# Kernel tuning notes

Hardware: AMD Instinct MI355X
Metric: run time of the kernel (lower is better)

Reference implementation:

```python
import jax, jax.numpy as jnp
import numpy as np

EPS = 1e-8
LRELU_SLOPE = 0.2
ACT_GAIN = float(np.sqrt(2.0))  # def_gain for lrelu
GAIN = 1.0                      # forward default
CLAMP = 256.0


def setup_inputs() -> dict:
    key = jax.random.key(0)
    k1, k2 = jax.random.split(key)
    x = jax.random.normal(k1, (8, 128, 32, 32, 32), dtype=jnp.float32)
    weight = jax.random.normal(k2, (128, 128, 3, 3, 3), dtype=jnp.float32)
    bias = jnp.zeros((128,), dtype=jnp.float32)
    return {"x": x, "weight": weight, "bias": bias}


def _modulated_conv3d(x, weight, styles, padding, demodulate=True):
    # x: [B, Cin, D, H, W], weight: [Cout, Cin, kd, kh, kw], styles: [B, Cin]
    w = weight[None] * styles[:, None, :, None, None, None]  # [B, Cout, Cin, kd, kh, kw]
    if demodulate:
        dcoefs = jax.lax.rsqrt(jnp.sum(jnp.square(w), axis=(2, 3, 4, 5)) + EPS)  # [B, Cout]
        w = w * dcoefs[:, :, None, None, None, None]
    pad = [(padding, padding)] * 3

    def per_sample(xi, wi):
        # xi: [Cin, D, H, W], wi: [Cout, Cin, kd, kh, kw]
        return jax.lax.conv_general_dilated(
            xi[None], wi, window_strides=(1, 1, 1), padding=pad,
            dimension_numbers=("NCDHW", "OIDHW", "NCDHW"))[0]

    return jax.vmap(per_sample)(x, w)  # [B, Cout, D, H, W]


def reference(x, weight, bias):
    padding = weight.shape[-1] // 2
    styles = jnp.ones((x.shape[0], weight.shape[1]), dtype=x.dtype)
    y = _modulated_conv3d(x, weight, styles, padding)
    y = jax.nn.leaky_relu(y + bias[None, :, None, None, None], LRELU_SLOPE)
    # clamp_gain(act, act_gain*gain, 256*gain)
    return jnp.clip(y * (ACT_GAIN * GAIN), -CLAMP * GAIN, CLAMP * GAIN)
```

## Files before the change

### kernel.cpp

```cpp
#include <hip/hip_runtime.h>

typedef short bf16x8 __attribute__((ext_vector_type(8)));
typedef float f32x4  __attribute__((ext_vector_type(4)));
typedef unsigned short u16;

static __device__ __forceinline__ u16 f2bf(float f) {
    unsigned int u = __builtin_bit_cast(unsigned int, f);
    u += 0x7FFFu + ((u >> 16) & 1u);
    return (u16)(u >> 16);
}

static __device__ __forceinline__ void gload_lds16(const void* g, void* l) {
    __builtin_amdgcn_global_load_lds((const __attribute__((address_space(1))) void*)g,
                                     (__attribute__((address_space(3))) void*)l, 16, 0, 0);
}

__global__ __launch_bounds__(256) void prep_w_k(const float* __restrict__ w,
                                                u16* __restrict__ wn) {
    const int co = blockIdx.x;
    const int t  = threadIdx.x;
    const float* wc = w + co * 3456;
    float s = 0.f;
    for (int i = t; i < 3456; i += 256) { float v = wc[i]; s += v * v; }
#pragma unroll
    for (int off = 32; off; off >>= 1) s += __shfl_down(s, off);
    __shared__ float red[4];
    __shared__ float dsh;
    if ((t & 63) == 0) red[t >> 6] = s;
    __syncthreads();
    if (t == 0) dsh = rsqrtf(red[0] + red[1] + red[2] + red[3] + 1e-8f);
    __syncthreads();
    const float d = dsh;
    for (int i = t; i < 3456; i += 256) {
        int ci = i / 27, tap = i - ci * 27;
        float v = wc[i] * d;
        wn[((tap * 4 + (ci >> 5)) * 128 + co) * 32 + (ci & 31)] = f2bf(v);
    }
}

__global__ __launch_bounds__(256) void xpose_k(const float* __restrict__ x,
                                               u16* __restrict__ xt) {
    const int bid = blockIdx.x;
    const int b = bid >> 10, d = (bid >> 5) & 31, h = bid & 31;
    const int t = threadIdx.x;
    const int w = t & 31, cg = t >> 5;
    const int base_dhw = d * 1024 + h * 32 + w;
#pragma unroll
    for (int r = 0; r < 2; ++r) {
        int g = cg + r * 8;
        const float* src = x + ((size_t)(b * 128 + g * 8) << 15) + base_dhw;
        bf16x8 pk;
#pragma unroll
        for (int j = 0; j < 8; ++j) pk[j] = (short)f2bf(src[(size_t)j << 15]);
        *(bf16x8*)&xt[((size_t)((b * 16 + g) << 15) + base_dhw) * 8] = pk;
    }
}

#define KSX 1048576
#define KSW 4096
#define RB  12288
__global__ __launch_bounds__(512, 4) void conv_mx(
    const u16* __restrict__ wsb, const float* __restrict__ bias,
    float* __restrict__ out) {
    __shared__ __align__(16) u16 lds[3 * RB];
    const u16* xt = wsb + 524288;
    const u16* wn = wsb + 512;
    const u16* zp = wsb;

    const int t = threadIdx.x, lane = t & 63, wid = t >> 6;
    const int ll = lane & 15, g = lane >> 4;
    const int mslice = wid >> 1, ncol = wid & 1;

    int wg = ((blockIdx.x & 7) << 7) | (blockIdx.x >> 3);
    const int b = wg >> 7, dt = (wg >> 3) & 15, ht = wg & 7;
    const int d0 = dt * 2, h0 = ht * 4;

    const int pos0 = mslice * 64 + ll;
    const int xro = pos0 * 32 + ((g ^ ((pos0 >> 1) & 3)) * 8);
    const int co0 = ncol * 64 + ll;
    const int wro = co0 * 32 + ((g ^ ((co0 >> 1) & 3)) * 8);

    const int posA = wid * 32 + (lane >> 2);
    const int slot = lane & 3;
    const int pdA = posA >> 7, phA = (posA >> 5) & 3, wA = posA & 31;
    const int gA = slot ^ ((posA >> 1) & 3);
    const int wco = wid * 16 + (lane >> 2);
    const u16* wsrc = wn + wco * 32 + ((slot ^ ((wco >> 1) & 3)) * 8);

    f32x4 acc[4][4];
#pragma unroll
    for (int i = 0; i < 4; ++i)
#pragma unroll
        for (int j = 0; j < 4; ++j) acc[i][j] = (f32x4){0.f, 0.f, 0.f, 0.f};

    int od_s = 0, oh_s = 0, ow_s = 0, cc_s = 0;
    const u16* xsA = xt; bool okA = false, okB = false;

#define DO_STAGE(SB) { \
    if (cc_s == 0) { \
        int Dx = d0 + pdA - 1 + od_s, Hx = h0 + phA - 1 + oh_s, Wx = wA - 1 + ow_s; \
        bool dh_ = ((unsigned)Dx < 32u) && ((unsigned)Hx < 32u); \
        okA = dh_ && ((unsigned)Wx < 32u); \
        okB = dh_ && (Wx < 16); \
        xsA = xt + (long)((b * 16 + gA) * 32768 + Dx * 1024 + Hx * 32 + Wx) * 8; } \
    gload_lds16(okA ? (const void*)xsA : (const void*)zp, (void*)&lds[(SB)*RB + wid*1024]); \
    gload_lds16(okB ? (const void*)(xsA + 128) : (const void*)zp, (void*)&lds[(SB)*RB + wid*1024 + 512]); \
    gload_lds16((const void*)wsrc, (void*)&lds[(SB)*RB + 8192 + wid*512]); \
    xsA += KSX; wsrc += KSW; \
    if (++cc_s == 4) { cc_s = 0; \
        if (++ow_s == 3) { ow_s = 0; if (++oh_s == 3) { oh_s = 0; ++od_s; } } } }

#define KSTEP(CB, SB, VMN, DOST) { \
    asm volatile("s_waitcnt vmcnt(" #VMN ")" ::: "memory"); \
    asm volatile("s_barrier" ::: "memory"); \
    bf16x8 xf[4], wf[4]; \
    _Pragma("unroll") for (int mf = 0; mf < 4; ++mf) \
        xf[mf] = *(const bf16x8*)&lds[(CB)*RB + xro + mf*512]; \
    _Pragma("unroll") for (int nf = 0; nf < 4; ++nf) \
        wf[nf] = *(const bf16x8*)&lds[(CB)*RB + 8192 + wro + nf*512]; \
    if (DOST) DO_STAGE(SB); \
    __builtin_amdgcn_s_setprio(1); \
    _Pragma("unroll") for (int mf = 0; mf < 4; ++mf) \
    _Pragma("unroll") for (int nf = 0; nf < 4; ++nf) \
        acc[mf][nf] = __builtin_amdgcn_mfma_f32_16x16x32_bf16(wf[nf], xf[mf], acc[mf][nf], 0, 0, 0); \
    __builtin_amdgcn_s_setprio(0); }

    DO_STAGE(0);
    DO_STAGE(1);

    for (int m = 0; m < 35; ++m) {
        KSTEP(0, 2, 3, 1);
        KSTEP(1, 0, 3, 1);
        KSTEP(2, 1, 3, 1);
    }
    KSTEP(0, 2, 3, 1);
    KSTEP(1, 0, 3, 0);
    KSTEP(2, 0, 0, 0);

    const int pd = mslice >> 1, phb = (mslice & 1) * 2;
#pragma unroll
    for (int nf = 0; nf < 4; ++nf) {
        f32x4 bb = *(const f32x4*)&bias[ncol * 64 + nf * 16 + g * 4];
#pragma unroll
        for (int mf = 0; mf < 4; ++mf) {
            const int wq = (mf & 1) * 16 + ll;
            const int hh = h0 + phb + (mf >> 1);
            float* orow = out + ((size_t)(b * 128 + ncol * 64 + nf * 16 + g * 4) << 15)
                          + (d0 + pd) * 1024 + hh * 32 + wq;
#pragma unroll
            for (int q = 0; q < 4; ++q) {
                float v = acc[mf][nf][q] + bb[q];
                v = v > 0.f ? v : v * 0.2f;
                v *= 1.41421356237f;
                v = fminf(fmaxf(v, -256.f), 256.f);
                orow[(size_t)q << 15] = v;
            }
        }
    }
#undef DO_STAGE
#undef KSTEP
}

#define NPOS 544
__global__ __launch_bounds__(256, 4) void conv_fb(
    const float* __restrict__ x, const u16* __restrict__ wn,
    const float* __restrict__ bias, float* __restrict__ out) {
    __shared__ __align__(16) u16 lds[NPOS * 32];
    float* ldsf = reinterpret_cast<float*>(lds);
    const int t = threadIdx.x;
    const int lane = t & 63;
    const int wid  = t >> 6;
    const int wr   = wid >> 1;
    const int wcn  = wid & 1;
    const int ll   = lane & 15;
    const int g    = lane >> 4;
    const int bid = blockIdx.x;
    const int b  = bid >> 8;
    const int dt = (bid >> 4) & 15, ht = bid & 15;
    const int d0 = dt * 2, h0 = ht * 2;
    const int sw  = t & 31;
    const int sg  = (t >> 5) & 3;
    const int rhi = t >> 7;
    f32x4 acc[4][4];
#pragma unroll
    for (int i = 0; i < 4; ++i)
#pragma unroll
        for (int j = 0; j < 4; ++j) acc[i][j] = (f32x4){0.f, 0.f, 0.f, 0.f};
    float bv[4][4];
#pragma unroll
    for (int nf = 0; nf < 4; ++nf) {
        f32x4 bb = *(const f32x4*)&bias[wcn * 64 + nf * 16 + g * 4];
#pragma unroll
        for (int q = 0; q < 4; ++q) bv[nf][q] = bb[q];
    }
    if (t < 128) {
        int pi  = t >> 2;
        int row = pi >> 1;
        int pos = row * 34 + (pi & 1) * 33;
        bf16x8 z = {0, 0, 0, 0, 0, 0, 0, 0};
        *(bf16x8*)&lds[pos * 32 + (t & 3) * 8] = z;
    }
    for (int c = 0; c < 4; ++c) {
        if (c) __syncthreads();
#pragma unroll
        for (int p = 0; p < 8; ++p) {
            int rowid = p * 2 + rhi;
            int pd = rowid >> 2, ph = rowid & 3;
            int d = d0 - 1 + pd, h = h0 - 1 + ph;
            bool ok = ((unsigned)d < 32u) && ((unsigned)h < 32u);
            const float* src = x + (((b * 128 + c * 32 + sg * 8) * 32 + d) * 32 + h) * 32 + sw;
            float v[8];
#pragma unroll
            for (int j = 0; j < 8; ++j) v[j] = ok ? src[j * 32768] : 0.f;
            bf16x8 pk;
#pragma unroll
            for (int j = 0; j < 8; ++j) pk[j] = (short)f2bf(v[j]);
            int pos = rowid * 34 + sw + 1;
            int sl = sg ^ ((pos >> 1) & 3);
            *(bf16x8*)&lds[pos * 32 + sl * 8] = pk;
        }
        __syncthreads();
        const u16* wbase = wn + c * 4096 + ((wcn * 64 + ll) * 32 + g * 8);
        bf16x8 wf[4];
#pragma unroll
        for (int nf = 0; nf < 4; ++nf) wf[nf] = *(const bf16x8*)&wbase[nf * 512];
#pragma unroll
        for (int tap = 0; tap < 27; ++tap) {
            const int od = tap / 9, oh = (tap / 3) % 3, ow = tap % 3;
            bf16x8 wfn[4];
            if (tap < 26) {
#pragma unroll
                for (int nf = 0; nf < 4; ++nf)
                    wfn[nf] = *(const bf16x8*)&wbase[(tap + 1) * 16384 + nf * 512];
            }
            bf16x8 xf[4];
#pragma unroll
            for (int mf = 0; mf < 4; ++mf) {
                int pos = ((wr + od) * 4 + (mf >> 1) + oh) * 34 + (mf & 1) * 16 + ll + ow;
                int sl = g ^ ((pos >> 1) & 3);
                xf[mf] = *(const bf16x8*)&lds[pos * 32 + sl * 8];
            }
            __builtin_amdgcn_s_setprio(1);
#pragma unroll
            for (int mf = 0; mf < 4; ++mf)
#pragma unroll
                for (int nf = 0; nf < 4; ++nf)
                    acc[mf][nf] = __builtin_amdgcn_mfma_f32_16x16x32_bf16(
                        wf[nf], xf[mf], acc[mf][nf], 0, 0, 0);
            __builtin_amdgcn_s_setprio(0);
            if (tap < 26) {
#pragma unroll
                for (int nf = 0; nf < 4; ++nf) wf[nf] = wfn[nf];
            }
        }
    }
#pragma unroll
    for (int p = 0; p < 4; ++p) {
        const int dd = p >> 1, hh = p & 1;
        __syncthreads();
        if (wr == dd) {
#pragma unroll
            for (int whalf = 0; whalf < 2; ++whalf) {
                const int mf = hh * 2 + whalf;
#pragma unroll
                for (int nf = 0; nf < 4; ++nf) {
#pragma unroll
                    for (int q = 0; q < 4; ++q) {
                        const int co = wcn * 64 + nf * 16 + g * 4 + q;
                        float v = acc[mf][nf][q] + bv[nf][q];
                        v = v > 0.f ? v : v * 0.2f;
                        v *= 1.41421356237f;
                        v = fminf(fmaxf(v, -256.f), 256.f);
                        ldsf[co * 33 + whalf * 16 + ll] = v;
                    }
                }
            }
        }
        __syncthreads();
#pragma unroll
        for (int it = 0; it < 4; ++it) {
            const int row = it * 32 + (t >> 3);
            const int ls  = t & 7;
            f32x4 v = *(f32x4*)&ldsf[row * 33 + ls * 4];
            *(f32x4*)&out[(size_t)(b * 128 + row) * 32768 +
                          (d0 + dd) * 1024 + (h0 + hh) * 32 + ls * 4] = v;
        }
    }
}

extern "C" void kernel_launch(void* const* d_in, const int* in_sizes, int n_in,
                              void* d_out, int out_size, void* d_ws, size_t ws_size,
                              hipStream_t stream) {
    const float* x    = (const float*)d_in[0];
    const float* w    = (const float*)d_in[1];
    const float* bias = (const float*)d_in[2];
    float* out        = (float*)d_out;
    u16* wsb          = (u16*)d_ws;

    hipMemsetAsync(d_ws, 0, 1024, stream);
    prep_w_k<<<128, 256, 0, stream>>>(w, wsb + 512);

    if (ws_size >= 68157440ull) {
        xpose_k<<<8192, 256, 0, stream>>>(x, wsb + 524288);
        conv_mx<<<1024, 512, 0, stream>>>(wsb, bias, out);
    } else {
        conv_fb<<<2048, 256, 0, stream>>>(x, wsb + 512, bias, out);
    }
}
```

Before: 296.2 us.

## Halve conv block to 4 waves with 128x64 per-wave tiles and post-MFMA barrier

Cuts the conv workgroup from 8 waves to 4. Each wave now computes 128 positions by 64 output channels (8x4 MFMA tiles), so fragment reuse from LDS rises and the number of LDS reads per MFMA falls. Each thread issues six global-to-LDS loads per stage instead of three. The wait and barrier move to after the MFMAs so the next stage's loads overlap compute. In exchange, accumulator registers double (128 floats), occupancy drops, and the swizzle and index math are rewritten.

```diff
diff --git a/kernel.cpp b/kernel.cpp
--- a/kernel.cpp
+++ b/kernel.cpp
@@ -59,7 +59,7 @@
 #define KSX 1048576
 #define KSW 4096
 #define RB  12288
-__global__ __launch_bounds__(512, 4) void conv_mx(
+__global__ __launch_bounds__(256, 2) void conv_mx(
     const u16* __restrict__ wsb, const float* __restrict__ bias,
     float* __restrict__ out) {
     __shared__ __align__(16) u16 lds[3 * RB];
@@ -75,78 +75,85 @@
     const int b = wg >> 7, dt = (wg >> 3) & 15, ht = wg & 7;
     const int d0 = dt * 2, h0 = ht * 4;
 
-    const int pos0 = mslice * 64 + ll;
-    const int xro = pos0 * 32 + ((g ^ ((pos0 >> 1) & 3)) * 8);
-    const int co0 = ncol * 64 + ll;
-    const int wro = co0 * 32 + ((g ^ ((co0 >> 1) & 3)) * 8);
-
-    const int posA = wid * 32 + (lane >> 2);
-    const int slot = lane & 3;
-    const int pdA = posA >> 7, phA = (posA >> 5) & 3, wA = posA & 31;
-    const int gA = slot ^ ((posA >> 1) & 3);
-    const int wco = wid * 16 + (lane >> 2);
-    const u16* wsrc = wn + wco * 32 + ((slot ^ ((wco >> 1) & 3)) * 8);
-
-    f32x4 acc[4][4];
-#pragma unroll
-    for (int i = 0; i < 4; ++i)
+    const int slotr = g ^ ((ll >> 1) & 3);
+    const int xro = (mslice * 128 + ll) * 32 + slotr * 8;
+    const int wro = 8192 + (ncol * 64 + ll) * 32 + slotr * 8;
+
+    const int gA = (lane & 3) ^ ((lane >> 3) & 3);
+    int pdl[4], phl[4], pwl[4];
+#pragma unroll
+    for (int i = 0; i < 4; ++i) {
+        int p = (wid * 4 + i) * 16 + (lane >> 2);
+        pdl[i] = p >> 7; phl[i] = (p >> 5) & 3; pwl[i] = p & 31;
+    }
+    const u16* wsrc0 = wn + ((wid * 2) * 16 + (lane >> 2)) * 32 + gA * 8;
+    const u16* wsrc1 = wsrc0 + 512;
+
+    f32x4 acc[8][4];
+#pragma unroll
+    for (int i = 0; i < 8; ++i)
 #pragma unroll
         for (int j = 0; j < 4; ++j) acc[i][j] = (f32x4){0.f, 0.f, 0.f, 0.f};
 
     int od_s = 0, oh_s = 0, ow_s = 0, cc_s = 0;
-    const u16* xsA = xt; bool okA = false, okB = false;
+    const u16* xs[4]; int okl[4];
 
 #define DO_STAGE(SB) { \
     if (cc_s == 0) { \
-        int Dx = d0 + pdA - 1 + od_s, Hx = h0 + phA - 1 + oh_s, Wx = wA - 1 + ow_s; \
-        bool dh_ = ((unsigned)Dx < 32u) && ((unsigned)Hx < 32u); \
-        okA = dh_ && ((unsigned)Wx < 32u); \
-        okB = dh_ && (Wx < 16); \
-        xsA = xt + (long)((b * 16 + gA) * 32768 + Dx * 1024 + Hx * 32 + Wx) * 8; } \
-    gload_lds16(okA ? (const void*)xsA : (const void*)zp, (void*)&lds[(SB)*RB + wid*1024]); \
-    gload_lds16(okB ? (const void*)(xsA + 128) : (const void*)zp, (void*)&lds[(SB)*RB + wid*1024 + 512]); \
-    gload_lds16((const void*)wsrc, (void*)&lds[(SB)*RB + 8192 + wid*512]); \
-    xsA += KSX; wsrc += KSW; \
+        _Pragma("unroll") for (int i = 0; i < 4; ++i) { \
+            int Dx = d0 + pdl[i] - 1 + od_s, Hx = h0 + phl[i] - 1 + oh_s, Wx = pwl[i] - 1 + ow_s; \
+            okl[i] = (((unsigned)Dx < 32u) && ((unsigned)Hx < 32u) && ((unsigned)Wx < 32u)) ? 1 : 0; \
+            xs[i] = xt + (long)((b * 16 + gA) * 32768 + Dx * 1024 + Hx * 32 + Wx) * 8; } } \
+    _Pragma("unroll") for (int i = 0; i < 4; ++i) \
+        gload_lds16(okl[i] ? (const void*)xs[i] : (const void*)zp, \
+                    (void*)&lds[(SB)*RB + (wid * 4 + i) * 512]); \
+    gload_lds16((const void*)wsrc0, (void*)&lds[(SB)*RB + 8192 + wid * 1024]); \
+    gload_lds16((const void*)wsrc1, (void*)&lds[(SB)*RB + 8192 + wid * 1024 + 512]); \
+    _Pragma("unroll") for (int i = 0; i < 4; ++i) xs[i] += KSX; \
+    wsrc0 += KSW; wsrc1 += KSW; \
     if (++cc_s == 4) { cc_s = 0; \
         if (++ow_s == 3) { ow_s = 0; if (++oh_s == 3) { oh_s = 0; ++od_s; } } } }
 
-#define KSTEP(CB, SB, VMN, DOST) { \
-    asm volatile("s_waitcnt vmcnt(" #VMN ")" ::: "memory"); \
-    asm volatile("s_barrier" ::: "memory"); \
-    bf16x8 xf[4], wf[4]; \
-    _Pragma("unroll") for (int mf = 0; mf < 4; ++mf) \
-        xf[mf] = *(const bf16x8*)&lds[(CB)*RB + xro + mf*512]; \
+#define KSTEP(CB, SB, DOST, VMSTR, DOBAR) { \
+    bf16x8 wf[4], xf[8]; \
     _Pragma("unroll") for (int nf = 0; nf < 4; ++nf) \
-        wf[nf] = *(const bf16x8*)&lds[(CB)*RB + 8192 + wro + nf*512]; \
+        wf[nf] = *(const bf16x8*)&lds[(CB)*RB + wro + nf * 512]; \
+    _Pragma("unroll") for (int mf = 0; mf < 8; ++mf) \
+        xf[mf] = *(const bf16x8*)&lds[(CB)*RB + xro + mf * 512]; \
     if (DOST) DO_STAGE(SB); \
     __builtin_amdgcn_s_setprio(1); \
-    _Pragma("unroll") for (int mf = 0; mf < 4; ++mf) \
+    _Pragma("unroll") for (int mf = 0; mf < 8; ++mf) \
     _Pragma("unroll") for (int nf = 0; nf < 4; ++nf) \
         acc[mf][nf] = __builtin_amdgcn_mfma_f32_16x16x32_bf16(wf[nf], xf[mf], acc[mf][nf], 0, 0, 0); \
-    __builtin_amdgcn_s_setprio(0); }
+    __builtin_amdgcn_s_setprio(0); \
+    if (DOBAR) { \
+        asm volatile("s_waitcnt " VMSTR ::: "memory"); \
+        asm volatile("s_barrier" ::: "memory"); } }
 
     DO_STAGE(0);
     DO_STAGE(1);
+    asm volatile("s_waitcnt vmcnt(6)" ::: "memory");
+    asm volatile("s_barrier" ::: "memory");
 
     for (int m = 0; m < 35; ++m) {
-        KSTEP(0, 2, 3, 1);
-        KSTEP(1, 0, 3, 1);
-        KSTEP(2, 1, 3, 1);
-    }
-    KSTEP(0, 2, 3, 1);
-    KSTEP(1, 0, 3, 0);
-    KSTEP(2, 0, 0, 0);
-
-    const int pd = mslice >> 1, phb = (mslice & 1) * 2;
+        KSTEP(0, 2, 1, "vmcnt(6)", 1);
+        KSTEP(1, 0, 1, "vmcnt(6)", 1);
+        KSTEP(2, 1, 1, "vmcnt(6)", 1);
+    }
+    KSTEP(0, 2, 1, "vmcnt(6)", 1);
+    KSTEP(1, 0, 0, "vmcnt(0)", 1);
+    KSTEP(2, 0, 0, "vmcnt(0)", 0);
+
+    const int dd = d0 + mslice;
 #pragma unroll
     for (int nf = 0; nf < 4; ++nf) {
         f32x4 bb = *(const f32x4*)&bias[ncol * 64 + nf * 16 + g * 4];
 #pragma unroll
-        for (int mf = 0; mf < 4; ++mf) {
+        for (int mf = 0; mf < 8; ++mf) {
             const int wq = (mf & 1) * 16 + ll;
-            const int hh = h0 + phb + (mf >> 1);
+            const int hh = h0 + (mf >> 1);
             float* orow = out + ((size_t)(b * 128 + ncol * 64 + nf * 16 + g * 4) << 15)
-                          + (d0 + pd) * 1024 + hh * 32 + wq;
+                          + dd * 1024 + hh * 32 + wq;
 #pragma unroll
             for (int q = 0; q < 4; ++q) {
                 float v = acc[mf][nf][q] + bb[q];
@@ -302,7 +309,7 @@
 
     if (ws_size >= 68157440ull) {
         xpose_k<<<8192, 256, 0, stream>>>(x, wsb + 524288);
-        conv_mx<<<1024, 512, 0, stream>>>(wsb, bias, out);
+        conv_mx<<<1024, 256, 0, stream>>>(wsb, bias, out);
     } else {
         conv_fb<<<2048, 256, 0, stream>>>(x, wsb + 512, bias, out);
     }
```

Result: no change. 292.8 us (-1.1%).

## Load conv weights directly to registers with double buffering instead of via LDS

Applied to the files above, without the earlier changes.

Weight fragments are now read straight from global memory into registers, double-buffered one K-step ahead, rather than being staged through LDS. This shrinks the LDS ring buffer to hold only activations, which cuts LDS traffic and footprint. The K-step is also restructured to split the activation LDS reads into two halves interleaved with MFMA groups, and the wait and barrier move to the end of each step. In exchange, every wave now issues its own global weight loads, which relies on L1/L2 hits, and register pressure rises.

```diff
diff --git a/kernel.cpp b/kernel.cpp
--- a/kernel.cpp
+++ b/kernel.cpp
@@ -57,8 +57,7 @@
 }
 
 #define KSX 1048576
-#define KSW 4096
-#define RB  12288
+#define RB  8192
 __global__ __launch_bounds__(512, 4) void conv_mx(
     const u16* __restrict__ wsb, const float* __restrict__ bias,
     float* __restrict__ out) {
@@ -77,15 +76,13 @@
 
     const int pos0 = mslice * 64 + ll;
     const int xro = pos0 * 32 + ((g ^ ((pos0 >> 1) & 3)) * 8);
-    const int co0 = ncol * 64 + ll;
-    const int wro = co0 * 32 + ((g ^ ((co0 >> 1) & 3)) * 8);
+
+    const u16* wptr = wn + (ncol * 64 + ll) * 32 + g * 8;
 
     const int posA = wid * 32 + (lane >> 2);
     const int slot = lane & 3;
     const int pdA = posA >> 7, phA = (posA >> 5) & 3, wA = posA & 31;
     const int gA = slot ^ ((posA >> 1) & 3);
-    const int wco = wid * 16 + (lane >> 2);
-    const u16* wsrc = wn + wco * 32 + ((slot ^ ((wco >> 1) & 3)) * 8);
 
     f32x4 acc[4][4];
 #pragma unroll
@@ -95,6 +92,13 @@
 
     int od_s = 0, oh_s = 0, ow_s = 0, cc_s = 0;
     const u16* xsA = xt; bool okA = false, okB = false;
+
+    bf16x8 wa[4], wb[4];
+
+#define WLOAD(WF) { \
+    _Pragma("unroll") for (int nf = 0; nf < 4; ++nf) \
+        WF[nf] = *(const bf16x8*)&wptr[nf * 512]; \
+    wptr += 4096; }
 
 #define DO_STAGE(SB) { \
     if (cc_s == 0) { \
@@ -105,37 +109,64 @@
         xsA = xt + (long)((b * 16 + gA) * 32768 + Dx * 1024 + Hx * 32 + Wx) * 8; } \
     gload_lds16(okA ? (const void*)xsA : (const void*)zp, (void*)&lds[(SB)*RB + wid*1024]); \
     gload_lds16(okB ? (const void*)(xsA + 128) : (const void*)zp, (void*)&lds[(SB)*RB + wid*1024 + 512]); \
-    gload_lds16((const void*)wsrc, (void*)&lds[(SB)*RB + 8192 + wid*512]); \
-    xsA += KSX; wsrc += KSW; \
+    xsA += KSX; \
     if (++cc_s == 4) { cc_s = 0; \
         if (++ow_s == 3) { ow_s = 0; if (++oh_s == 3) { oh_s = 0; ++od_s; } } } }
 
-#define KSTEP(CB, SB, VMN, DOST) { \
-    asm volatile("s_waitcnt vmcnt(" #VMN ")" ::: "memory"); \
-    asm volatile("s_barrier" ::: "memory"); \
-    bf16x8 xf[4], wf[4]; \
-    _Pragma("unroll") for (int mf = 0; mf < 4; ++mf) \
-        xf[mf] = *(const bf16x8*)&lds[(CB)*RB + xro + mf*512]; \
-    _Pragma("unroll") for (int nf = 0; nf < 4; ++nf) \
-        wf[nf] = *(const bf16x8*)&lds[(CB)*RB + 8192 + wro + nf*512]; \
-    if (DOST) DO_STAGE(SB); \
+#define KSTEP(RD, SB, CW, NW, DOST, DOW, VMSTR) { \
+    if (DOW) { WLOAD(NW); } \
+    bf16x8 xf0 = *(const bf16x8*)&lds[(RD)*RB + xro]; \
+    bf16x8 xf1 = *(const bf16x8*)&lds[(RD)*RB + xro + 512]; \
+    if (DOST) { DO_STAGE(SB); } \
     __builtin_amdgcn_s_setprio(1); \
-    _Pragma("unroll") for (int mf = 0; mf < 4; ++mf) \
-    _Pragma("unroll") for (int nf = 0; nf < 4; ++nf) \
-        acc[mf][nf] = __builtin_amdgcn_mfma_f32_16x16x32_bf16(wf[nf], xf[mf], acc[mf][nf], 0, 0, 0); \
-    __builtin_amdgcn_s_setprio(0); }
-
-    DO_STAGE(0);
-    DO_STAGE(1);
-
-    for (int m = 0; m < 35; ++m) {
-        KSTEP(0, 2, 3, 1);
-        KSTEP(1, 0, 3, 1);
-        KSTEP(2, 1, 3, 1);
-    }
-    KSTEP(0, 2, 3, 1);
-    KSTEP(1, 0, 3, 0);
-    KSTEP(2, 0, 0, 0);
+    _Pragma("unroll") for (int nf = 0; nf < 4; ++nf) \
+        acc[0][nf] = __builtin_amdgcn_mfma_f32_16x16x32_bf16(CW[nf], xf0, acc[0][nf], 0, 0, 0); \
+    _Pragma("unroll") for (int nf = 0; nf < 4; ++nf) \
+        acc[1][nf] = __builtin_amdgcn_mfma_f32_16x16x32_bf16(CW[nf], xf1, acc[1][nf], 0, 0, 0); \
+    __builtin_amdgcn_s_setprio(0); \
+    bf16x8 xf2 = *(const bf16x8*)&lds[(RD)*RB + xro + 1024]; \
+    bf16x8 xf3 = *(const bf16x8*)&lds[(RD)*RB + xro + 1536]; \
+    __builtin_amdgcn_s_setprio(1); \
+    _Pragma("unroll") for (int nf = 0; nf < 4; ++nf) \
+        acc[2][nf] = __builtin_amdgcn_mfma_f32_16x16x32_bf16(CW[nf], xf2, acc[2][nf], 0, 0, 0); \
+    _Pragma("unroll") for (int nf = 0; nf < 4; ++nf) \
+        acc[3][nf] = __builtin_amdgcn_mfma_f32_16x16x32_bf16(CW[nf], xf3, acc[3][nf], 0, 0, 0); \
+    __builtin_amdgcn_s_setprio(0); \
+    asm volatile("s_waitcnt lgkmcnt(0)" ::: "memory"); \
+    asm volatile("s_waitcnt " VMSTR ::: "memory"); \
+    asm volatile("s_barrier" ::: "memory"); }
+
+    DO_STAGE(0); DO_STAGE(1);
+    WLOAD(wa);
+    asm volatile("s_waitcnt vmcnt(6)" ::: "memory");
+    asm volatile("s_barrier" ::: "memory");
+
+    for (int m = 0; m < 17; ++m) {
+        KSTEP(0, 2, wa, wb, 1, 1, "vmcnt(6)");
+        KSTEP(1, 0, wb, wa, 1, 1, "vmcnt(6)");
+        KSTEP(2, 1, wa, wb, 1, 1, "vmcnt(6)");
+        KSTEP(0, 2, wb, wa, 1, 1, "vmcnt(6)");
+        KSTEP(1, 0, wa, wb, 1, 1, "vmcnt(6)");
+        KSTEP(2, 1, wb, wa, 1, 1, "vmcnt(6)");
+    }
+    KSTEP(0, 2, wa, wb, 1, 1, "vmcnt(6)");
+    KSTEP(1, 0, wb, wa, 1, 1, "vmcnt(6)");
+    KSTEP(2, 1, wa, wb, 1, 1, "vmcnt(6)");
+    KSTEP(0, 2, wb, wa, 1, 1, "vmcnt(6)");
+    KSTEP(1, 0, wa, wb, 0, 1, "vmcnt(4)");
+    {
+        bf16x8 xf0 = *(const bf16x8*)&lds[2 * RB + xro];
+        bf16x8 xf1 = *(const bf16x8*)&lds[2 * RB + xro + 512];
+        bf16x8 xf2 = *(const bf16x8*)&lds[2 * RB + xro + 1024];
+        bf16x8 xf3 = *(const bf16x8*)&lds[2 * RB + xro + 1536];
+#pragma unroll
+        for (int nf = 0; nf < 4; ++nf) {
+            acc[0][nf] = __builtin_amdgcn_mfma_f32_16x16x32_bf16(wb[nf], xf0, acc[0][nf], 0, 0, 0);
+            acc[1][nf] = __builtin_amdgcn_mfma_f32_16x16x32_bf16(wb[nf], xf1, acc[1][nf], 0, 0, 0);
+            acc[2][nf] = __builtin_amdgcn_mfma_f32_16x16x32_bf16(wb[nf], xf2, acc[2][nf], 0, 0, 0);
+            acc[3][nf] = __builtin_amdgcn_mfma_f32_16x16x32_bf16(wb[nf], xf3, acc[3][nf], 0, 0, 0);
+        }
+    }
 
     const int pd = mslice >> 1, phb = (mslice & 1) * 2;
 #pragma unroll
@@ -157,6 +188,7 @@
             }
         }
     }
+#undef WLOAD
 #undef DO_STAGE
 #undef KSTEP
 }
```

After: 696.0 us. 135% more time.

## Replace tap-streamed implicit GEMM with halo-tile LDS reuse across all 27 taps

Applied to the files above, without the earlier changes.

The conv kernel is restructured. Instead of streaming one shifted input slice per (tap, channel chunk) into a triple-buffered LDS pipeline, each block now loads a padded halo tile (4 rows × 34 columns) per 32-channel chunk into LDS once. It then reuses that tile for all 27 taps, reading weights directly from global memory. This cuts redundant global/L2 input traffic roughly 27x per chunk, at the cost of losing the async multi-stage overlap (plain syncthreads around each load) and putting weight loads in the MFMA loop. The block size also drops to 256 threads with 2048 blocks.

```diff
diff --git a/kernel.cpp b/kernel.cpp
--- a/kernel.cpp
+++ b/kernel.cpp
@@ -56,13 +56,11 @@
     }
 }
 
-#define KSX 1048576
-#define KSW 4096
-#define RB  12288
-__global__ __launch_bounds__(512, 4) void conv_mx(
+#define NPOS 544
+__global__ __launch_bounds__(256, 4) void conv_hx(
     const u16* __restrict__ wsb, const float* __restrict__ bias,
     float* __restrict__ out) {
-    __shared__ __align__(16) u16 lds[3 * RB];
+    __shared__ __align__(16) u16 lds[NPOS * 32];
     const u16* xt = wsb + 524288;
     const u16* wn = wsb + 512;
     const u16* zp = wsb;
@@ -71,21 +69,13 @@
     const int ll = lane & 15, g = lane >> 4;
     const int mslice = wid >> 1, ncol = wid & 1;
 
-    int wg = ((blockIdx.x & 7) << 7) | (blockIdx.x >> 3);
-    const int b = wg >> 7, dt = (wg >> 3) & 15, ht = wg & 7;
-    const int d0 = dt * 2, h0 = ht * 4;
-
-    const int pos0 = mslice * 64 + ll;
-    const int xro = pos0 * 32 + ((g ^ ((pos0 >> 1) & 3)) * 8);
-    const int co0 = ncol * 64 + ll;
-    const int wro = co0 * 32 + ((g ^ ((co0 >> 1) & 3)) * 8);
-
-    const int posA = wid * 32 + (lane >> 2);
-    const int slot = lane & 3;
-    const int pdA = posA >> 7, phA = (posA >> 5) & 3, wA = posA & 31;
-    const int gA = slot ^ ((posA >> 1) & 3);
-    const int wco = wid * 16 + (lane >> 2);
-    const u16* wsrc = wn + wco * 32 + ((slot ^ ((wco >> 1) & 3)) * 8);
+    int wg = ((blockIdx.x & 7) << 8) | (blockIdx.x >> 3);
+    const int b = wg >> 8, dt = (wg >> 4) & 15, ht = wg & 15;
+    const int d0 = dt * 2, h0 = ht * 2;
+
+    const int sstart = (wid < 2) ? wid * 9 : 18 + (wid - 2) * 8;
+    const int scount = (wid < 2) ? 9 : 8;
+    const int lhi = lane >> 2, slotl = lane & 3;
 
     f32x4 acc[4][4];
 #pragma unroll
@@ -93,60 +83,62 @@
 #pragma unroll
         for (int j = 0; j < 4; ++j) acc[i][j] = (f32x4){0.f, 0.f, 0.f, 0.f};
 
-    int od_s = 0, oh_s = 0, ow_s = 0, cc_s = 0;
-    const u16* xsA = xt; bool okA = false, okB = false;
-
-#define DO_STAGE(SB) { \
-    if (cc_s == 0) { \
-        int Dx = d0 + pdA - 1 + od_s, Hx = h0 + phA - 1 + oh_s, Wx = wA - 1 + ow_s; \
-        bool dh_ = ((unsigned)Dx < 32u) && ((unsigned)Hx < 32u); \
-        okA = dh_ && ((unsigned)Wx < 32u); \
-        okB = dh_ && (Wx < 16); \
-        xsA = xt + (long)((b * 16 + gA) * 32768 + Dx * 1024 + Hx * 32 + Wx) * 8; } \
-    gload_lds16(okA ? (const void*)xsA : (const void*)zp, (void*)&lds[(SB)*RB + wid*1024]); \
-    gload_lds16(okB ? (const void*)(xsA + 128) : (const void*)zp, (void*)&lds[(SB)*RB + wid*1024 + 512]); \
-    gload_lds16((const void*)wsrc, (void*)&lds[(SB)*RB + 8192 + wid*512]); \
-    xsA += KSX; wsrc += KSW; \
-    if (++cc_s == 4) { cc_s = 0; \
-        if (++ow_s == 3) { ow_s = 0; if (++oh_s == 3) { oh_s = 0; ++od_s; } } } }
-
-#define KSTEP(CB, SB, VMN, DOST) { \
-    asm volatile("s_waitcnt vmcnt(" #VMN ")" ::: "memory"); \
-    asm volatile("s_barrier" ::: "memory"); \
-    bf16x8 xf[4], wf[4]; \
-    _Pragma("unroll") for (int mf = 0; mf < 4; ++mf) \
-        xf[mf] = *(const bf16x8*)&lds[(CB)*RB + xro + mf*512]; \
-    _Pragma("unroll") for (int nf = 0; nf < 4; ++nf) \
-        wf[nf] = *(const bf16x8*)&lds[(CB)*RB + 8192 + wro + nf*512]; \
-    if (DOST) DO_STAGE(SB); \
-    __builtin_amdgcn_s_setprio(1); \
-    _Pragma("unroll") for (int mf = 0; mf < 4; ++mf) \
-    _Pragma("unroll") for (int nf = 0; nf < 4; ++nf) \
-        acc[mf][nf] = __builtin_amdgcn_mfma_f32_16x16x32_bf16(wf[nf], xf[mf], acc[mf][nf], 0, 0, 0); \
-    __builtin_amdgcn_s_setprio(0); }
-
-    DO_STAGE(0);
-    DO_STAGE(1);
-
-    for (int m = 0; m < 35; ++m) {
-        KSTEP(0, 2, 3, 1);
-        KSTEP(1, 0, 3, 1);
-        KSTEP(2, 1, 3, 1);
-    }
-    KSTEP(0, 2, 3, 1);
-    KSTEP(1, 0, 3, 0);
-    KSTEP(2, 0, 0, 0);
-
-    const int pd = mslice >> 1, phb = (mslice & 1) * 2;
+    for (int c = 0; c < 4; ++c) {
+        __syncthreads();
+        for (int i = 0; i < scount; ++i) {
+            int ai  = sstart + i;
+            int pos = ai * 16 + lhi;
+            int row = (pos * 964) >> 15;
+            int w1  = pos - row * 34;
+            int Dx  = d0 - 1 + (row >> 2);
+            int Hx  = h0 - 1 + (row & 3);
+            int W   = w1 - 1;
+            int gg  = slotl ^ ((pos >> 1) & 3);
+            bool ok = ((unsigned)Dx < 32u) && ((unsigned)Hx < 32u) &&
+                      ((unsigned)W < 32u);
+            const u16* src = xt + ((((size_t)(b * 16 + c * 4 + gg)) << 15)
+                                   + Dx * 1024 + Hx * 32 + W) * 8;
+            gload_lds16(ok ? (const void*)src : (const void*)zp,
+                        (void*)((char*)lds + ai * 1024));
+        }
+        __syncthreads();
+
+        const u16* wbase = wn + c * 4096 + ((ncol * 64 + ll) * 32 + g * 8);
+#pragma unroll
+        for (int tap = 0; tap < 27; ++tap) {
+            const int od = tap / 9, oh = (tap / 3) % 3, ow = tap % 3;
+            bf16x8 wf[4];
+#pragma unroll
+            for (int nf = 0; nf < 4; ++nf)
+                wf[nf] = *(const bf16x8*)&wbase[tap * 16384 + nf * 512];
+            bf16x8 xf[4];
+#pragma unroll
+            for (int mf = 0; mf < 4; ++mf) {
+                int pos = ((mslice + od) * 4 + (mf >> 1) + oh) * 34 +
+                          (mf & 1) * 16 + ll + ow;
+                int sl = g ^ ((pos >> 1) & 3);
+                xf[mf] = *(const bf16x8*)&lds[pos * 32 + sl * 8];
+            }
+            __builtin_amdgcn_s_setprio(1);
+#pragma unroll
+            for (int mf = 0; mf < 4; ++mf)
+#pragma unroll
+                for (int nf = 0; nf < 4; ++nf)
+                    acc[mf][nf] = __builtin_amdgcn_mfma_f32_16x16x32_bf16(
+                        wf[nf], xf[mf], acc[mf][nf], 0, 0, 0);
+            __builtin_amdgcn_s_setprio(0);
+        }
+    }
+
 #pragma unroll
     for (int nf = 0; nf < 4; ++nf) {
         f32x4 bb = *(const f32x4*)&bias[ncol * 64 + nf * 16 + g * 4];
 #pragma unroll
         for (int mf = 0; mf < 4; ++mf) {
             const int wq = (mf & 1) * 16 + ll;
-            const int hh = h0 + phb + (mf >> 1);
+            const int hh = h0 + (mf >> 1);
             float* orow = out + ((size_t)(b * 128 + ncol * 64 + nf * 16 + g * 4) << 15)
-                          + (d0 + pd) * 1024 + hh * 32 + wq;
+                          + (d0 + mslice) * 1024 + hh * 32 + wq;
 #pragma unroll
             for (int q = 0; q < 4; ++q) {
                 float v = acc[mf][nf][q] + bb[q];
@@ -157,11 +149,8 @@
             }
         }
     }
-#undef DO_STAGE
-#undef KSTEP
-}
-
-#define NPOS 544
+}
+
 __global__ __launch_bounds__(256, 4) void conv_fb(
     const float* __restrict__ x, const u16* __restrict__ wn,
     const float* __restrict__ bias, float* __restrict__ out) {
@@ -302,7 +291,7 @@
 
     if (ws_size >= 68157440ull) {
         xpose_k<<<8192, 256, 0, stream>>>(x, wsb + 524288);
-        conv_mx<<<1024, 512, 0, stream>>>(wsb, bias, out);
+        conv_hx<<<2048, 256, 0, stream>>>(wsb, bias, out);
     } else {
         conv_fb<<<2048, 256, 0, stream>>>(x, wsb + 512, bias, out);
     }
```

Result: slower. 403.3 us (+36.2%).
